# Kernel tuning notes

Hardware: AMD Instinct MI355X
Metric: run time of the kernel (lower is better)

## Reference

```python
import jax, jax.numpy as jnp
import numpy as np

N, E, IN, HID, OUT = 50000, 800000, 128, 96, 2


def setup_inputs() -> dict:
    key = jax.random.key(0)
    ks = jax.random.split(key, 10)
    x = jax.random.normal(ks[0], (N, IN), jnp.float32)
    edge_index = jax.random.randint(ks[1], (2, E), 0, N, dtype=jnp.int64)
    # PQVA mask: per-node, first output channel is a "known" quantity (masked out),
    # second is the prediction target -> ~mask selects exactly N elements.
    m = np.zeros((N, OUT), dtype=bool)
    m[:, 0] = True
    PQVA_mask = jnp.asarray(m)
    scaler_mean = 0.1 * jax.random.normal(ks[2], (IN,), jnp.float32)
    scaler_std = 0.5 + jax.random.uniform(ks[3], (IN,), jnp.float32)  # in [0.5, 1.5)
    W1 = jax.random.normal(ks[4], (IN, HID), jnp.float32) / np.sqrt(IN)
    W2 = jax.random.normal(ks[5], (HID, HID), jnp.float32) / np.sqrt(HID)
    W3 = jax.random.normal(ks[6], (HID, HID), jnp.float32) / np.sqrt(HID)
    Wout = jax.random.normal(ks[7], (HID, OUT), jnp.float32) / np.sqrt(HID)
    b1 = jnp.zeros((HID,), jnp.float32)
    b2 = jnp.zeros((HID,), jnp.float32)
    b3 = jnp.zeros((HID,), jnp.float32)
    bout = jnp.zeros((OUT,), jnp.float32)
    return {"x": x, "edge_index": edge_index, "PQVA_mask": PQVA_mask,
            "scaler_mean": scaler_mean, "scaler_std": scaler_std,
            "W1": W1, "b1": b1, "W2": W2, "b2": b2, "W3": W3, "b3": b3,
            "Wout": Wout, "bout": bout}


def reference(x, edge_index, PQVA_mask, scaler_mean, scaler_std,
              W1, b1, W2, b2, W3, b3, Wout, bout):
    n = x.shape[0]
    loop = jnp.arange(n, dtype=edge_index.dtype)
    src = jnp.concatenate([edge_index[0], loop])  # add self-loops (GCNConv default)
    dst = jnp.concatenate([edge_index[1], loop])
    deg = jax.ops.segment_sum(jnp.ones_like(dst, x.dtype), dst, num_segments=n)
    dinv = jax.lax.rsqrt(deg)  # deg >= 1 thanks to self-loops
    norm = (dinv[src] * dinv[dst])[:, None]  # [E+N, 1]

    def prop(h):  # D^-1/2 (A+I) D^-1/2 @ h  via gather-scale-scatter
        return jax.ops.segment_sum(h[src] * norm, dst, num_segments=n)

    h = (x - scaler_mean) / scaler_std          # standard scaler
    h = jax.nn.relu(prop(h @ W1) + b1)          # GCNConv 1 + ReLU
    h = jax.nn.relu(prop(h @ W2) + b2)          # GCNConv 2 + ReLU
    h = prop(h @ W3) + b3                       # GCNConv 3 (last, no act)
    out = h @ Wout + bout                       # final Linear -> [N, OUT]
    # masked reshape: ~mask has exactly one True per node -> [N]
    return out.reshape(-1)[~PQVA_mask.reshape(-1)]
```

## Files before the change

kernel.cpp:

```cpp
#include <hip/hip_runtime.h>
#include <hip/hip_fp16.h>

#define IN_F 128
#define HID_F 96
#define PB 512
#define STRIDE 6144
#define MAXB 8192

typedef _Float16 f16x8 __attribute__((ext_vector_type(8)));
typedef float f32x4 __attribute__((ext_vector_type(4)));

__device__ __forceinline__ void swizzle_one(const float* W, __half* Wsw, int idx) {
    int j  = idx & 7;
    int ln = (idx >> 3) & 63;
    int ct = idx >> 9;
    int t = ct % 6, c = ct / 6;
    int k   = c * 32 + (ln >> 4) * 8 + j;
    int col = t * 16 + (ln & 15);
    Wsw[idx] = (__half)W[k * 96 + col];
}

__global__ __launch_bounds__(256) void part_prep_kernel(
        const int* __restrict__ srcv, const int* __restrict__ dstv,
        int* __restrict__ bcur, int* __restrict__ ebuf, int E,
        const float* __restrict__ stdv, float* __restrict__ rstd,
        const float* __restrict__ W3, const float* __restrict__ Wout,
        const float* __restrict__ b3, const float* __restrict__ bout,
        float* __restrict__ wv, float* __restrict__ cconst,
        const float* __restrict__ W1, __half* __restrict__ Wsw1, int SW1,
        const float* __restrict__ W2, __half* __restrict__ Wsw2, int SW2) {
    int b = blockIdx.x, t = threadIdx.x;
    if (b >= PB) {
        int pb = b - PB;
        if (pb == 0) {
            if (t < IN_F) rstd[t] = 1.0f / stdv[t];
            if (t < HID_F) {
                float s = 0.f;
                for (int j = 0; j < HID_F; ++j) s += W3[t * HID_F + j] * Wout[j * 2 + 1];
                wv[t] = s;
            }
            if (t == 0) {
                float s = 0.f;
                for (int j = 0; j < HID_F; ++j) s += b3[j] * Wout[j * 2 + 1];
                cconst[0] = s + bout[1];
            }
        } else if (pb <= 48) {
            int idx = (pb - 1) * 256 + t;
            if (idx < SW1) swizzle_one(W1, Wsw1, idx);
        } else {
            int idx = (pb - 49) * 256 + t;
            if (idx < SW2) swizzle_one(W2, Wsw2, idx);
        }
        return;
    }
    __shared__ int h[256];
    __shared__ int cur[256];
    int chunk = (E + PB - 1) / PB;
    int s = b * chunk;
    int eend = min(s + chunk, E);
    h[t] = 0;
    __syncthreads();
    for (int e = s + t; e < eend; e += 256) atomicAdd(&h[dstv[e] >> 8], 1);
    __syncthreads();
    if (h[t]) cur[t] = t * STRIDE + atomicAdd(&bcur[t], h[t]);
    __syncthreads();
    for (int e = s + t; e < eend; e += 256) {
        int sv = srcv[e], d = dstv[e];
        int p = atomicAdd(&cur[d >> 8], 1);
        ebuf[p] = (sv << 8) | (d & 255);
    }
}


template<int MODE, int K, int SC>
__device__ __forceinline__ void gemm_body(
        int bid, int tid,
        const void* __restrict__ Ain, const __half* __restrict__ Wsw,
        const float* __restrict__ mean, const float* __restrict__ rstd,
        const float* __restrict__ dinv, __half* __restrict__ C, int n) {
    constexpr int NCH = K / 32;
    int lane = tid & 63;
    int wv_  = tid >> 6;
    int m = lane & 15, q = lane >> 4;
    int node0 = bid * 64 + wv_ * 16;
    int g = node0 + m;
    int gc = g < n ? g : n - 1;

    f32x4 acc[6];
#pragma unroll
    for (int t = 0; t < 6; ++t) acc[t] = (f32x4){0.f, 0.f, 0.f, 0.f};

#pragma unroll
    for (int c = 0; c < NCH; ++c) {
        f16x8 a;
        if (MODE == 0) {
            const float* ap = (const float*)Ain + (long)gc * K + c * 32 + q * 8;
            float4 v0 = *(const float4*)ap;
            float4 v1 = *(const float4*)(ap + 4);
            float4 m0 = *(const float4*)(mean + c * 32 + q * 8);
            float4 m1 = *(const float4*)(mean + c * 32 + q * 8 + 4);
            float4 r0 = *(const float4*)(rstd + c * 32 + q * 8);
            float4 r1 = *(const float4*)(rstd + c * 32 + q * 8 + 4);
            a[0] = (_Float16)((v0.x - m0.x) * r0.x);
            a[1] = (_Float16)((v0.y - m0.y) * r0.y);
            a[2] = (_Float16)((v0.z - m0.z) * r0.z);
            a[3] = (_Float16)((v0.w - m0.w) * r0.w);
            a[4] = (_Float16)((v1.x - m1.x) * r1.x);
            a[5] = (_Float16)((v1.y - m1.y) * r1.y);
            a[6] = (_Float16)((v1.z - m1.z) * r1.z);
            a[7] = (_Float16)((v1.w - m1.w) * r1.w);
        } else {
            a = *(const f16x8*)((const __half*)Ain + (long)gc * K + c * 32 + q * 8);
        }
#pragma unroll
        for (int t = 0; t < 6; ++t) {
            f16x8 b = *(const f16x8*)(Wsw + (size_t)(((c * 6) + t) * 64 + lane) * 8);
            acc[t] = __builtin_amdgcn_mfma_f32_16x16x32_f16(a, b, acc[t], 0, 0, 0);
        }
    }
    float dv[4];
#pragma unroll
    for (int r = 0; r < 4; ++r) {
        int gr = node0 + q * 4 + r;
        dv[r] = SC ? ((gr < n) ? dinv[gr] : 0.f) : 1.f;
    }
#pragma unroll
    for (int t = 0; t < 6; ++t)
#pragma unroll
        for (int r = 0; r < 4; ++r) {
            int gr = node0 + q * 4 + r;
            float o = SC ? acc[t][r] * dv[r] : acc[t][r];
            if (gr < n) C[(long)gr * 96 + t * 16 + m] = (__half)o;
        }
}

template<int MODE, int K, int SC>
__global__ __launch_bounds__(256) void gemm_mfma_kernel(
        const void* __restrict__ Ain, const __half* __restrict__ Wsw,
        const float* __restrict__ mean, const float* __restrict__ rstd,
        const float* __restrict__ dinv, __half* __restrict__ C, int n) {
    gemm_body<MODE, K, SC>(blockIdx.x, threadIdx.x, Ain, Wsw, mean, rstd, dinv, C, n);
}


__global__ __launch_bounds__(256) void csr_gemm1_kernel(
        const int* __restrict__ ebuf, const int* __restrict__ bcur,
        int* __restrict__ rowdeg, float* __restrict__ dinv,
        int* __restrict__ cols, int n, int nb,
        const float* __restrict__ x, const __half* __restrict__ Wsw1,
        const float* __restrict__ mean, const float* __restrict__ rstd,
        __half* __restrict__ C) {
    __shared__ int dg[256];
    __shared__ int tmp[256];
    __shared__ int cur[256];
    __shared__ int colst[MAXB];
    int t = threadIdx.x;
    if (blockIdx.x >= nb) {
        gemm_body<0, IN_F, 0>(blockIdx.x - nb, t, x, Wsw1, mean, rstd, nullptr, C, n);
        return;
    }
    int k = blockIdx.x;
    int seg = k * STRIDE;
    int cnt = min(bcur[k], STRIDE);
    dg[t] = 0;
    __syncthreads();
    for (int i = t; i < cnt; i += 256) atomicAdd(&dg[ebuf[seg + i] & 255], 1);
    __syncthreads();
    int v = dg[t];
    tmp[t] = v;
    __syncthreads();
#pragma unroll
    for (int off = 1; off < 256; off <<= 1) {
        int u = (t >= off) ? tmp[t - off] : 0;
        __syncthreads();
        tmp[t] += u;
        __syncthreads();
    }
    int excl = tmp[t] - v;
    int node = (k << 8) + t;
    if (node < n) {
        rowdeg[node] = ((seg + excl) << 9) | v;
        dinv[node] = rsqrtf((float)v + 1.0f);
    }
    cur[t] = excl;
    __syncthreads();
    for (int i = t; i < cnt; i += 256) {
        int p = ebuf[seg + i];
        int lp = atomicAdd(&cur[p & 255], 1);
        colst[lp] = ((unsigned)p) >> 8;
    }
    __syncthreads();
    for (int i = t; i < cnt; i += 256) cols[seg + i] = colst[i];
}


template<int DOT, int SCALE>
__global__ __launch_bounds__(256) void prop16_kernel(
        const __half* __restrict__ hin, const int* __restrict__ rowdeg,
        const int* __restrict__ cols,
        const float* __restrict__ dinv, const float* __restrict__ bias,
        const float* __restrict__ wvv, __half* __restrict__ hout,
        float* __restrict__ zs, int n) {
    int wid = (blockIdx.x * blockDim.x + threadIdx.x) >> 6;
    int lane = threadIdx.x & 63;
    if (wid >= n) return;
    int rd = rowdeg[wid];
    int e0 = ((unsigned)rd) >> 9;
    int deg = rd & 511;
    float di = dinv[wid];
    bool active = lane < 48;
    int g = lane / 12, l = lane - g * 12;
    int gg = active ? g : 0;
    const f16x8* hp = (const f16x8*)hin;

    int colv = cols[e0 + lane];
    f16x8 vself = hp[(long)wid * 12 + l];

    float acc[8];
    float sself = (g == 0) ? (SCALE ? di : 1.f) : 0.f;
#pragma unroll
    for (int j = 0; j < 8; ++j) acc[j] = sself * (float)vself[j];

    int dcap = deg < 64 ? deg : 64;
    int e = 0;
    for (; e + 16 <= dcap; e += 16) {
        int p = e + gg;
        int c0 = __shfl(colv, p, 64);
        int c1 = __shfl(colv, p + 4, 64);
        int c2 = __shfl(colv, p + 8, 64);
        int c3 = __shfl(colv, p + 12, 64);
        float s0 = 1.f, s1 = 1.f, s2 = 1.f, s3 = 1.f;
        if (SCALE) { s0 = dinv[c0]; s1 = dinv[c1]; s2 = dinv[c2]; s3 = dinv[c3]; }
        f16x8 v0 = hp[(long)c0 * 12 + l];
        f16x8 v1 = hp[(long)c1 * 12 + l];
        f16x8 v2 = hp[(long)c2 * 12 + l];
        f16x8 v3 = hp[(long)c3 * 12 + l];
#pragma unroll
        for (int j = 0; j < 8; ++j) {
            acc[j] = fmaf((float)v0[j], s0, acc[j]);
            acc[j] = fmaf((float)v1[j], s1, acc[j]);
            acc[j] = fmaf((float)v2[j], s2, acc[j]);
            acc[j] = fmaf((float)v3[j], s3, acc[j]);
        }
    }
    for (; e < dcap; e += 4) {
        int idx = e + gg;
        bool is = active && idx < dcap;
        int cs = __shfl(colv, idx & 63, 64);
        int c = is ? cs : wid;
        f16x8 v = hp[(long)c * 12 + l];
        float sc = SCALE ? dinv[c] : 1.f;
        float s = is ? sc : 0.f;
#pragma unroll
        for (int j = 0; j < 8; ++j) acc[j] = fmaf((float)v[j], s, acc[j]);
    }
    for (int ee = 64; ee < deg; ee += 4) {
        int idx = ee + gg;
        bool is = active && idx < deg;
        int c = is ? cols[e0 + idx] : wid;
        f16x8 v = hp[(long)c * 12 + l];
        float sc = SCALE ? dinv[c] : 1.f;
        float s = is ? sc : 0.f;
#pragma unroll
        for (int j = 0; j < 8; ++j) acc[j] = fmaf((float)v[j], s, acc[j]);
    }
#pragma unroll
    for (int j = 0; j < 8; ++j) {
        acc[j] += __shfl_down(acc[j], 24, 64);
        acc[j] += __shfl_down(acc[j], 12, 64);
    }
    if (DOT == 0) {
        if (lane < 12) {
            float4 b0 = *(const float4*)(bias + lane * 8);
            float4 b1 = *(const float4*)(bias + lane * 8 + 4);
            f16x8 o;
            o[0] = (_Float16)fmaxf(di * acc[0] + b0.x, 0.f);
            o[1] = (_Float16)fmaxf(di * acc[1] + b0.y, 0.f);
            o[2] = (_Float16)fmaxf(di * acc[2] + b0.z, 0.f);
            o[3] = (_Float16)fmaxf(di * acc[3] + b0.w, 0.f);
            o[4] = (_Float16)fmaxf(di * acc[4] + b1.x, 0.f);
            o[5] = (_Float16)fmaxf(di * acc[5] + b1.y, 0.f);
            o[6] = (_Float16)fmaxf(di * acc[6] + b1.z, 0.f);
            o[7] = (_Float16)fmaxf(di * acc[7] + b1.w, 0.f);
            *(f16x8*)(hout + (long)wid * 96 + lane * 8) = o;
        }
    } else {
        float v = 0.f;
        if (lane < 12) {
            float4 b0 = *(const float4*)(bias + lane * 8);
            float4 b1 = *(const float4*)(bias + lane * 8 + 4);
            float4 w0 = *(const float4*)(wvv + lane * 8);
            float4 w1 = *(const float4*)(wvv + lane * 8 + 4);
            v  = fmaxf(di * acc[0] + b0.x, 0.f) * w0.x;
            v += fmaxf(di * acc[1] + b0.y, 0.f) * w0.y;
            v += fmaxf(di * acc[2] + b0.z, 0.f) * w0.z;
            v += fmaxf(di * acc[3] + b0.w, 0.f) * w0.w;
            v += fmaxf(di * acc[4] + b1.x, 0.f) * w1.x;
            v += fmaxf(di * acc[5] + b1.y, 0.f) * w1.y;
            v += fmaxf(di * acc[6] + b1.z, 0.f) * w1.z;
            v += fmaxf(di * acc[7] + b1.w, 0.f) * w1.w;
        }
#pragma unroll
        for (int off = 32; off; off >>= 1) v += __shfl_xor(v, off, 64);
        if (lane == 0) zs[wid] = di * v;
    }
}


__global__ __launch_bounds__(256) void prop_scalar_kernel(
        const float* __restrict__ zs, const int* __restrict__ rowdeg,
        const int* __restrict__ cols,
        const float* __restrict__ dinv, const float* __restrict__ cconst,
        float* __restrict__ out, int n) {
    int i = blockIdx.x * blockDim.x + threadIdx.x;
    if (i >= n) return;
    int rd = rowdeg[i];
    int e0 = ((unsigned)rd) >> 9;
    int e1 = e0 + (rd & 511);
    float s = 0.f;
    int e = e0;
    for (; e + 4 <= e1; e += 4) {
        int c0 = cols[e + 0], c1 = cols[e + 1], c2 = cols[e + 2], c3 = cols[e + 3];
        s += zs[c0]; s += zs[c1]; s += zs[c2]; s += zs[c3];
    }
    for (; e < e1; ++e) s += zs[cols[e]];
    out[i] = dinv[i] * (s + zs[i]) + cconst[0];
}


extern "C" void kernel_launch(void* const* d_in, const int* in_sizes, int n_in,
                              void* d_out, int out_size, void* d_ws, size_t ws_size,
                              hipStream_t stream) {
    const float* x    = (const float*)d_in[0];
    const int*   eidx = (const int*)d_in[1];
    const float* mean = (const float*)d_in[3];
    const float* stdv = (const float*)d_in[4];
    const float* W1   = (const float*)d_in[5];
    const float* b1   = (const float*)d_in[6];
    const float* W2   = (const float*)d_in[7];
    const float* b2   = (const float*)d_in[8];
    const float* W3   = (const float*)d_in[9];
    const float* b3   = (const float*)d_in[10];
    const float* Wout = (const float*)d_in[11];
    const float* bout = (const float*)d_in[12];
    float* out = (float*)d_out;

    const int n = in_sizes[0] / IN_F;
    const int E = in_sizes[1] / 2;
    const int* srcv = eidx;
    const int* dstv = eidx + E;
    const int NB = (n + 255) >> 8;

    char* ws = (char*)d_ws;
    size_t off = 0;
    auto alloc = [&](size_t bytes) -> void* {
        void* p = ws + off;
        off = (off + bytes + 255) & ~(size_t)255;
        return p;
    };
    const int SW1 = 4 * 6 * 64 * 8;
    const int SW2 = 3 * 6 * 64 * 8;
    int*    rowdeg = (int*)alloc((size_t)n * 4);
    float*  dinv   = (float*)alloc((size_t)n * 4);
    int*    cols   = (int*)alloc((size_t)256 * STRIDE * 4);
    int*    ebuf   = (int*)alloc((size_t)256 * STRIDE * 4);
    int*    bcur   = (int*)alloc(256 * 4);
    float*  rstd   = (float*)alloc(IN_F * 4);
    float*  wv     = (float*)alloc(HID_F * 4);
    float*  cconst = (float*)alloc(4);
    float*  zbuf   = (float*)alloc((size_t)n * 4);
    __half* Wsw1   = (__half*)alloc((size_t)SW1 * 2);
    __half* Wsw2   = (__half*)alloc((size_t)SW2 * 2);
    __half* bufA   = (__half*)alloc((size_t)n * HID_F * 2);
    __half* bufB   = (__half*)alloc((size_t)n * HID_F * 2);

    hipMemsetAsync(bcur, 0, 256 * 4, stream);

    part_prep_kernel<<<PB + 85, 256, 0, stream>>>(
        srcv, dstv, bcur, ebuf, E,
        stdv, rstd, W3, Wout, b3, bout, wv, cconst,
        W1, Wsw1, SW1, W2, Wsw2, SW2);

    int gemm_grid = (n + 63) / 64;
    int prop_grid = (int)(((long)n * 64 + 255) / 256);

    csr_gemm1_kernel<<<NB + gemm_grid, 256, 0, stream>>>(
        ebuf, bcur, rowdeg, dinv, cols, n, NB, x, Wsw1, mean, rstd, bufA);

    prop16_kernel<0, 1><<<prop_grid, 256, 0, stream>>>(bufA, rowdeg, cols, dinv, b1,
                                                       nullptr, bufB, nullptr, n);
    gemm_mfma_kernel<1, HID_F, 1><<<gemm_grid, 256, 0, stream>>>(
        bufB, Wsw2, nullptr, nullptr, dinv, bufA, n);
    prop16_kernel<1, 0><<<prop_grid, 256, 0, stream>>>(bufA, rowdeg, cols, dinv, b2,
                                                       wv, nullptr, zbuf, n);
    prop_scalar_kernel<<<(n + 255) / 256, 256, 0, stream>>>(zbuf, rowdeg, cols, dinv,
                                                            cconst, out, n);
}
```

Baseline: 200.6 us.

## Map four nodes per wavefront in GCN propagation instead of one

The propagation kernel previously gave each 64-lane wavefront one node, with 48 active lanes split into 4 edge groups that were reduced at the end. Now each wavefront handles four nodes, each with a 16-lane group (12 active lanes over 96 fp16 features). Each group loads its column indices in chunks of 16 and walks its own edges, so the cross-group reduction goes away and 4x fewer waves are launched. With about 17 edges per node this should improve lane utilisation. The cost is divergence between the four nodes' degrees inside a wave and a quarter of the lanes sitting idle.

```diff
diff --git a/kernel.cpp b/kernel.cpp
--- a/kernel.cpp
+++ b/kernel.cpp
@@ -195,84 +195,68 @@
 
 
 template<int DOT, int SCALE>
-__global__ __launch_bounds__(256) void prop16_kernel(
+__global__ __launch_bounds__(256) void prop4_kernel(
         const __half* __restrict__ hin, const int* __restrict__ rowdeg,
         const int* __restrict__ cols,
         const float* __restrict__ dinv, const float* __restrict__ bias,
         const float* __restrict__ wvv, __half* __restrict__ hout,
         float* __restrict__ zs, int n) {
-    int wid = (blockIdx.x * blockDim.x + threadIdx.x) >> 6;
+    int wid  = (blockIdx.x * blockDim.x + threadIdx.x) >> 6;
     int lane = threadIdx.x & 63;
-    if (wid >= n) return;
-    int rd = rowdeg[wid];
+    int g = lane >> 4;
+    int l = lane & 15;
+    int node = wid * 4 + g;
+    bool nvalid = node < n;
+    int nodec = nvalid ? node : n - 1;
+    int rd = rowdeg[nodec];
     int e0 = ((unsigned)rd) >> 9;
     int deg = rd & 511;
-    float di = dinv[wid];
-    bool active = lane < 48;
-    int g = lane / 12, l = lane - g * 12;
-    int gg = active ? g : 0;
+    float di = dinv[nodec];
     const f16x8* hp = (const f16x8*)hin;
-
-    int colv = cols[e0 + lane];
-    f16x8 vself = hp[(long)wid * 12 + l];
-
+    int lc = l < 12 ? l : 0;
+
+    f16x8 vself = hp[(long)nodec * 12 + lc];
+    float sself = SCALE ? di : 1.f;
     float acc[8];
-    float sself = (g == 0) ? (SCALE ? di : 1.f) : 0.f;
 #pragma unroll
     for (int j = 0; j < 8; ++j) acc[j] = sself * (float)vself[j];
 
-    int dcap = deg < 64 ? deg : 64;
-    int e = 0;
-    for (; e + 16 <= dcap; e += 16) {
-        int p = e + gg;
-        int c0 = __shfl(colv, p, 64);
-        int c1 = __shfl(colv, p + 4, 64);
-        int c2 = __shfl(colv, p + 8, 64);
-        int c3 = __shfl(colv, p + 12, 64);
-        float s0 = 1.f, s1 = 1.f, s2 = 1.f, s3 = 1.f;
-        if (SCALE) { s0 = dinv[c0]; s1 = dinv[c1]; s2 = dinv[c2]; s3 = dinv[c3]; }
-        f16x8 v0 = hp[(long)c0 * 12 + l];
-        f16x8 v1 = hp[(long)c1 * 12 + l];
-        f16x8 v2 = hp[(long)c2 * 12 + l];
-        f16x8 v3 = hp[(long)c3 * 12 + l];
-#pragma unroll
-        for (int j = 0; j < 8; ++j) {
-            acc[j] = fmaf((float)v0[j], s0, acc[j]);
-            acc[j] = fmaf((float)v1[j], s1, acc[j]);
-            acc[j] = fmaf((float)v2[j], s2, acc[j]);
-            acc[j] = fmaf((float)v3[j], s3, acc[j]);
-        }
-    }
-    for (; e < dcap; e += 4) {
-        int idx = e + gg;
-        bool is = active && idx < dcap;
-        int cs = __shfl(colv, idx & 63, 64);
-        int c = is ? cs : wid;
-        f16x8 v = hp[(long)c * 12 + l];
-        float sc = SCALE ? dinv[c] : 1.f;
-        float s = is ? sc : 0.f;
-#pragma unroll
-        for (int j = 0; j < 8; ++j) acc[j] = fmaf((float)v[j], s, acc[j]);
-    }
-    for (int ee = 64; ee < deg; ee += 4) {
-        int idx = ee + gg;
-        bool is = active && idx < deg;
-        int c = is ? cols[e0 + idx] : wid;
-        f16x8 v = hp[(long)c * 12 + l];
-        float sc = SCALE ? dinv[c] : 1.f;
-        float s = is ? sc : 0.f;
-#pragma unroll
-        for (int j = 0; j < 8; ++j) acc[j] = fmaf((float)v[j], s, acc[j]);
-    }
-#pragma unroll
-    for (int j = 0; j < 8; ++j) {
-        acc[j] += __shfl_down(acc[j], 24, 64);
-        acc[j] += __shfl_down(acc[j], 12, 64);
-    }
+    for (int eb = 0; eb < deg; eb += 16) {
+        int colv = cols[e0 + eb + l];
+        int rem = deg - eb;
+        if (rem > 16) rem = 16;
+#pragma unroll
+        for (int k0 = 0; k0 < 16; k0 += 4) {
+            if (k0 >= rem) break;
+            int c[4];
+            float s[4];
+#pragma unroll
+            for (int kk = 0; kk < 4; ++kk) {
+                int p = k0 + kk;
+                bool is = p < rem;
+                int cc = __shfl(colv, (g << 4) + p, 64);
+                c[kk] = is ? cc : nodec;
+                float sc = SCALE ? dinv[c[kk]] : 1.f;
+                s[kk] = is ? sc : 0.f;
+            }
+            f16x8 v0 = hp[(long)c[0] * 12 + lc];
+            f16x8 v1 = hp[(long)c[1] * 12 + lc];
+            f16x8 v2 = hp[(long)c[2] * 12 + lc];
+            f16x8 v3 = hp[(long)c[3] * 12 + lc];
+#pragma unroll
+            for (int j = 0; j < 8; ++j) {
+                acc[j] = fmaf((float)v0[j], s[0], acc[j]);
+                acc[j] = fmaf((float)v1[j], s[1], acc[j]);
+                acc[j] = fmaf((float)v2[j], s[2], acc[j]);
+                acc[j] = fmaf((float)v3[j], s[3], acc[j]);
+            }
+        }
+    }
+
     if (DOT == 0) {
-        if (lane < 12) {
-            float4 b0 = *(const float4*)(bias + lane * 8);
-            float4 b1 = *(const float4*)(bias + lane * 8 + 4);
+        if (nvalid && l < 12) {
+            float4 b0 = *(const float4*)(bias + l * 8);
+            float4 b1 = *(const float4*)(bias + l * 8 + 4);
             f16x8 o;
             o[0] = (_Float16)fmaxf(di * acc[0] + b0.x, 0.f);
             o[1] = (_Float16)fmaxf(di * acc[1] + b0.y, 0.f);
@@ -282,15 +266,15 @@
             o[5] = (_Float16)fmaxf(di * acc[5] + b1.y, 0.f);
             o[6] = (_Float16)fmaxf(di * acc[6] + b1.z, 0.f);
             o[7] = (_Float16)fmaxf(di * acc[7] + b1.w, 0.f);
-            *(f16x8*)(hout + (long)wid * 96 + lane * 8) = o;
+            *(f16x8*)(hout + (long)node * 96 + l * 8) = o;
         }
     } else {
         float v = 0.f;
-        if (lane < 12) {
-            float4 b0 = *(const float4*)(bias + lane * 8);
-            float4 b1 = *(const float4*)(bias + lane * 8 + 4);
-            float4 w0 = *(const float4*)(wvv + lane * 8);
-            float4 w1 = *(const float4*)(wvv + lane * 8 + 4);
+        if (l < 12) {
+            float4 b0 = *(const float4*)(bias + l * 8);
+            float4 b1 = *(const float4*)(bias + l * 8 + 4);
+            float4 w0 = *(const float4*)(wvv + l * 8);
+            float4 w1 = *(const float4*)(wvv + l * 8 + 4);
             v  = fmaxf(di * acc[0] + b0.x, 0.f) * w0.x;
             v += fmaxf(di * acc[1] + b0.y, 0.f) * w0.y;
             v += fmaxf(di * acc[2] + b0.z, 0.f) * w0.z;
@@ -300,9 +284,11 @@
             v += fmaxf(di * acc[6] + b1.z, 0.f) * w1.z;
             v += fmaxf(di * acc[7] + b1.w, 0.f) * w1.w;
         }
-#pragma unroll
-        for (int off = 32; off; off >>= 1) v += __shfl_xor(v, off, 64);
-        if (lane == 0) zs[wid] = di * v;
+        v += __shfl_xor(v, 1, 64);
+        v += __shfl_xor(v, 2, 64);
+        v += __shfl_xor(v, 4, 64);
+        v += __shfl_xor(v, 8, 64);
+        if (nvalid && l == 0) zs[node] = di * v;
     }
 }
 
@@ -382,17 +368,18 @@
         W1, Wsw1, SW1, W2, Wsw2, SW2);
 
     int gemm_grid = (n + 63) / 64;
-    int prop_grid = (int)(((long)n * 64 + 255) / 256);
+    int wpg = (n + 3) / 4;
+    int prop_grid = (int)(((long)wpg * 64 + 255) / 256);
 
     csr_gemm1_kernel<<<NB + gemm_grid, 256, 0, stream>>>(
         ebuf, bcur, rowdeg, dinv, cols, n, NB, x, Wsw1, mean, rstd, bufA);
 
-    prop16_kernel<0, 1><<<prop_grid, 256, 0, stream>>>(bufA, rowdeg, cols, dinv, b1,
-                                                       nullptr, bufB, nullptr, n);
+    prop4_kernel<0, 1><<<prop_grid, 256, 0, stream>>>(bufA, rowdeg, cols, dinv, b1,
+                                                      nullptr, bufB, nullptr, n);
     gemm_mfma_kernel<1, HID_F, 1><<<gemm_grid, 256, 0, stream>>>(
         bufB, Wsw2, nullptr, nullptr, dinv, bufA, n);
-    prop16_kernel<1, 0><<<prop_grid, 256, 0, stream>>>(bufA, rowdeg, cols, dinv, b2,
-                                                       wv, nullptr, zbuf, n);
+    prop4_kernel<1, 0><<<prop_grid, 256, 0, stream>>>(bufA, rowdeg, cols, dinv, b2,
+                                                      wv, nullptr, zbuf, n);
     prop_scalar_kernel<<<(n + 255) / 256, 256, 0, stream>>>(zbuf, rowdeg, cols, dinv,
                                                             cconst, out, n);
 }
```

New measurement: 197.0 us. About the same (-1.8%).
